# Performance work log

Hardware: AMD Instinct MI355X
Metric: run time of the kernel (lower is better)

Reference implementation:

```python
import jax, jax.numpy as jnp
import numpy as np

N, F_IN, H, OUT = 8192, 512, 128, 3
DEG_P = 16.0 / N  # avg degree ~16


def setup_inputs() -> dict:
    key = jax.random.key(0)
    ks = jax.random.split(key, 10)
    x = jax.random.normal(ks[0], (N, F_IN), dtype=jnp.float32)
    adj = (jax.random.uniform(ks[1], (N, N)) < DEG_P).astype(jnp.float32)

    def glorot(k, shape):
        lim = float(np.sqrt(6.0 / (shape[0] + shape[1])))
        return jax.random.uniform(k, shape, jnp.float32, -lim, lim)

    return {
        "x": x,
        "adj": adj,
        "Wl1": glorot(ks[2], (F_IN, H)),   # neighbor-agg weight, layer 1
        "Wr1": glorot(ks[3], (F_IN, H)),   # root/self weight, layer 1
        "b1": jnp.zeros((H,), jnp.float32),
        "Wl2": glorot(ks[4], (H, H)),
        "Wr2": glorot(ks[5], (H, H)),
        "b2": jnp.zeros((H,), jnp.float32),
        "Wd": glorot(ks[6], (H, OUT)),
        "bd": jnp.zeros((OUT,), jnp.float32),
    }


def _sage(x, adj, Wl, Wr, b):
    # GraphSAGE-mean: mean over neighbors via dense adjacency, then transform.
    deg = jnp.maximum(adj.sum(axis=1, keepdims=True), 1.0)  # [N,1]
    agg = (adj @ x) / deg                                    # [N,F]
    return agg @ Wl + x @ Wr + b


def _cdist(y):
    # pairwise Euclidean distances, grad-safe sqrt (zero grad on zero dist)
    sq = jnp.sum(y * y, axis=-1)                             # [N]
    d2 = jnp.maximum(sq[:, None] + sq[None, :] - 2.0 * (y @ y.T), 0.0)
    return jnp.where(d2 > 0, jnp.sqrt(jnp.where(d2 > 0, d2, 1.0)), 0.0)


def reference(x, adj, Wl1, Wr1, b1, Wl2, Wr2, b2, Wd, bd):
    h = jax.nn.relu(_sage(x, adj, Wl1, Wr1, b1))
    # dropout p=0.5 is identity in eval mode
    h = _sage(h, adj, Wl2, Wr2, b2)
    y = h @ Wd + bd                                          # [N,3]
    return _cdist(y)                                         # [N,N]
```

## Files before the change

### kernel.cpp

```cpp
#include <hip/hip_runtime.h>
#include <math.h>

#define NN 8192
#define FIN 512
#define HD 128
#define CAP 128
#define GEMM_B 512
#define ADJ_B  2048

__global__ __launch_bounds__(256) void k_front(
    const float* __restrict__ x, const float* __restrict__ Wl1,
    const float* __restrict__ Wr1, const float* __restrict__ adj,
    const float* __restrict__ Wl2, const float* __restrict__ Wr2,
    const float* __restrict__ b2, const float* __restrict__ Wd,
    const float* __restrict__ bd,
    float* __restrict__ xl, float* __restrict__ xr,
    int* __restrict__ nbr, int* __restrict__ degi, float* __restrict__ degf,
    float4* __restrict__ wsm)
{
    __shared__ float As[32][32];
    __shared__ float Bs[32][128];
    const int tid = threadIdx.x;

    if (blockIdx.x < GEMM_B) {
        const float* W = (blockIdx.x < 256) ? Wl1 : Wr1;
        float* Cout    = (blockIdx.x < 256) ? xl  : xr;
        const int row0 = (blockIdx.x & 255) * 32;
        const int rg = tid >> 5, cg = tid & 31;
        const int ar = tid >> 3, ak = (tid & 7) * 4;
        const int bk = tid >> 5, bc = (tid & 31) * 4;
        float acc[4][4] = {};
        for (int ch = 0; ch < FIN / 32; ++ch) {
            const int kc = ch * 32;
            __syncthreads();
            const float4 va = *(const float4*)(x + (size_t)(row0 + ar) * FIN + kc + ak);
            As[ak + 0][ar] = va.x; As[ak + 1][ar] = va.y;
            As[ak + 2][ar] = va.z; As[ak + 3][ar] = va.w;
            #pragma unroll
            for (int it = 0; it < 4; ++it)
                *(float4*)&Bs[bk + 8 * it][bc] =
                    *(const float4*)(W + (size_t)(kc + bk + 8 * it) * HD + bc);
            __syncthreads();
            #pragma unroll
            for (int k = 0; k < 32; ++k) {
                const float4 a4 = *(const float4*)&As[k][rg * 4];
                const float4 b4 = *(const float4*)&Bs[k][cg * 4];
                const float av[4] = {a4.x, a4.y, a4.z, a4.w};
                const float bv[4] = {b4.x, b4.y, b4.z, b4.w};
                #pragma unroll
                for (int a = 0; a < 4; ++a)
                    #pragma unroll
                    for (int b = 0; b < 4; ++b)
                        acc[a][b] = fmaf(av[a], bv[b], acc[a][b]);
            }
        }
        #pragma unroll
        for (int a = 0; a < 4; ++a)
            *(float4*)(Cout + (size_t)(row0 + rg * 4 + a) * HD + cg * 4) =
                make_float4(acc[a][0], acc[a][1], acc[a][2], acc[a][3]);
    } else if (blockIdx.x < GEMM_B + ADJ_B) {
        const int w = tid >> 6, lane = tid & 63;
        const int i = (blockIdx.x - GEMM_B) * 4 + w;
        int* lst = nbr + (size_t)i * CAP;
        const float4* row = (const float4*)(adj + (size_t)i * NN);
        const unsigned long long lmask = (1ull << lane) - 1ull;
        int cnt = 0;
        for (int it = 0; it < NN / 256; ++it) {
            const float4 a = row[it * 64 + lane];
            const float vals[4] = {a.x, a.y, a.z, a.w};
            #pragma unroll
            for (int e = 0; e < 4; ++e) {
                const bool nz = (vals[e] != 0.0f);
                const unsigned long long m = __ballot(nz);
                if (nz) {
                    const int p = cnt + (int)__popcll(m & lmask);
                    if (p < CAP) lst[p] = (it * 64 + lane) * 4 + e;
                }
                cnt += (int)__popcll(m);
            }
        }
        if (lane == 0) {
            degi[i] = cnt < CAP ? cnt : CAP;
            degf[i] = fmaxf((float)cnt, 1.0f);
        }
    } else {
        const int t = tid;
        if (t < HD) {
            float l0 = 0, l1 = 0, l2 = 0, r0 = 0, r1 = 0, r2 = 0;
            for (int c = 0; c < HD; ++c) {
                const float w0 = Wd[c * 3 + 0], w1 = Wd[c * 3 + 1], w2 = Wd[c * 3 + 2];
                const float wl = Wl2[t * HD + c];
                const float wr = Wr2[t * HD + c];
                l0 = fmaf(wl, w0, l0); l1 = fmaf(wl, w1, l1); l2 = fmaf(wl, w2, l2);
                r0 = fmaf(wr, w0, r0); r1 = fmaf(wr, w1, r1); r2 = fmaf(wr, w2, r2);
            }
            wsm[t]       = make_float4(l0, l1, l2, 0.f);
            wsm[128 + t] = make_float4(r0, r1, r2, 0.f);
            if (t == 0) {
                float c0 = bd[0], c1 = bd[1], c2 = bd[2];
                for (int c = 0; c < HD; ++c) {
                    c0 = fmaf(b2[c], Wd[c * 3 + 0], c0);
                    c1 = fmaf(b2[c], Wd[c * 3 + 1], c1);
                    c2 = fmaf(b2[c], Wd[c * 3 + 2], c2);
                }
                wsm[256] = make_float4(c0, c1, c2, 0.f);
            }
        }
    }
}

__global__ __launch_bounds__(256) void k_agg_proj(
    const float* __restrict__ xl, const float* __restrict__ xr,
    const float* __restrict__ b1, const int* __restrict__ nbr,
    const int* __restrict__ degi, const float* __restrict__ degf,
    const float4* __restrict__ wsm, float4* __restrict__ u4,
    float4* __restrict__ v4)
{
    __shared__ int lists[4][CAP];
    const int w = threadIdx.x >> 6, lane = threadIdx.x & 63;
    const int i = blockIdx.x * 4 + w;
    const int d = degi[i];
    const float inv = 1.0f / degf[i];
    const int* glst = nbr + (size_t)i * CAP;
    if (lane < d)      lists[w][lane]      = glst[lane];
    if (lane + 64 < d) lists[w][lane + 64] = glst[lane + 64];
    const int* lst = lists[w];

    float s0 = 0.f, s1 = 0.f;
    int t = 0;
    for (; t + 4 <= d; t += 4) {
        const int j0 = lst[t], j1 = lst[t + 1], j2 = lst[t + 2], j3 = lst[t + 3];
        const float2 a0 = ((const float2*)(xl + (size_t)j0 * HD))[lane];
        const float2 a1 = ((const float2*)(xl + (size_t)j1 * HD))[lane];
        const float2 a2 = ((const float2*)(xl + (size_t)j2 * HD))[lane];
        const float2 a3 = ((const float2*)(xl + (size_t)j3 * HD))[lane];
        s0 += a0.x + a1.x + a2.x + a3.x;
        s1 += a0.y + a1.y + a2.y + a3.y;
    }
    for (; t < d; ++t) {
        const float2 a0 = ((const float2*)(xl + (size_t)lst[t] * HD))[lane];
        s0 += a0.x; s1 += a0.y;
    }

    const float2 rr = ((const float2*)(xr + (size_t)i * HD))[lane];
    const float2 bb = ((const float2*)b1)[lane];
    const float h0 = fmaxf(fmaf(s0, inv, rr.x + bb.x), 0.f);
    const float h1 = fmaxf(fmaf(s1, inv, rr.y + bb.y), 0.f);
    const float4 w0 = wsm[2 * lane], w1 = wsm[2 * lane + 1];
    const float4 q0 = wsm[128 + 2 * lane], q1 = wsm[128 + 2 * lane + 1];
    float u0 = h0 * w0.x + h1 * w1.x;
    float u1 = h0 * w0.y + h1 * w1.y;
    float u2 = h0 * w0.z + h1 * w1.z;
    float v0 = h0 * q0.x + h1 * q1.x;
    float v1 = h0 * q0.y + h1 * q1.y;
    float v2 = h0 * q0.z + h1 * q1.z;
    #pragma unroll
    for (int off = 32; off; off >>= 1) {
        u0 += __shfl_xor(u0, off); u1 += __shfl_xor(u1, off); u2 += __shfl_xor(u2, off);
        v0 += __shfl_xor(v0, off); v1 += __shfl_xor(v1, off); v2 += __shfl_xor(v2, off);
    }
    if (lane == 0) {
        u4[i] = make_float4(u0, u1, u2, 0.f);
        v4[i] = make_float4(v0, v1, v2, 0.f);
    }
}

__global__ __launch_bounds__(256) void k_ycomb(
    const float4* __restrict__ u4, const float4* __restrict__ v4,
    const int* __restrict__ nbr, const int* __restrict__ degi,
    const float* __restrict__ degf, const float4* __restrict__ wsm,
    float4* __restrict__ y4)
{
    const int hw = threadIdx.x >> 5;
    const int lane = threadIdx.x & 31;
    const int i = blockIdx.x * 8 + hw;
    const int d = degi[i];
    const float inv = 1.0f / degf[i];
    const int* lst = nbr + (size_t)i * CAP;
    float s0 = 0.f, s1 = 0.f, s2 = 0.f;
    for (int base = 0; base + lane < d; base += 32) {
        const float4 u = u4[lst[base + lane]];
        s0 += u.x; s1 += u.y; s2 += u.z;
    }
    #pragma unroll
    for (int off = 16; off; off >>= 1) {
        s0 += __shfl_xor(s0, off); s1 += __shfl_xor(s1, off); s2 += __shfl_xor(s2, off);
    }
    if (lane == 0) {
        const float4 v = v4[i];
        const float4 c = wsm[256];
        y4[i] = make_float4(fmaf(s0, inv, v.x + c.x),
                            fmaf(s1, inv, v.y + c.y),
                            fmaf(s2, inv, v.z + c.z), 0.f);
    }
}

__global__ __launch_bounds__(256) void k_cdist(
    const float4* __restrict__ y4, float* __restrict__ out)
{
    __shared__ float4 yis[32];
    const int t = threadIdx.x;
    const int i0 = blockIdx.y * 32;
    if (t < 32) yis[t] = y4[i0 + t];
    __syncthreads();
    const int j0 = blockIdx.x * 1024 + t * 4;
    const float4 a0 = y4[j0 + 0], a1 = y4[j0 + 1];
    const float4 a2 = y4[j0 + 2], a3 = y4[j0 + 3];
    float* op = out + (size_t)i0 * NN + j0;
    #pragma unroll 4
    for (int ii = 0; ii < 32; ++ii) {
        const float4 yi = yis[ii];
        float4 r;
        { const float dx = yi.x - a0.x, dy = yi.y - a0.y, dz = yi.z - a0.z;
          r.x = sqrtf(fmaf(dx, dx, fmaf(dy, dy, dz * dz))); }
        { const float dx = yi.x - a1.x, dy = yi.y - a1.y, dz = yi.z - a1.z;
          r.y = sqrtf(fmaf(dx, dx, fmaf(dy, dy, dz * dz))); }
        { const float dx = yi.x - a2.x, dy = yi.y - a2.y, dz = yi.z - a2.z;
          r.z = sqrtf(fmaf(dx, dx, fmaf(dy, dy, dz * dz))); }
        { const float dx = yi.x - a3.x, dy = yi.y - a3.y, dz = yi.z - a3.z;
          r.w = sqrtf(fmaf(dx, dx, fmaf(dy, dy, dz * dz))); }
        *(float4*)op = r;
        op += NN;
    }
}

extern "C" void kernel_launch(void* const* d_in, const int* in_sizes, int n_in,
                              void* d_out, int out_size, void* d_ws, size_t ws_size,
                              hipStream_t stream) {
    const float* x   = (const float*)d_in[0];
    const float* adj = (const float*)d_in[1];
    const float* Wl1 = (const float*)d_in[2];
    const float* Wr1 = (const float*)d_in[3];
    const float* b1  = (const float*)d_in[4];
    const float* Wl2 = (const float*)d_in[5];
    const float* Wr2 = (const float*)d_in[6];
    const float* b2  = (const float*)d_in[7];
    const float* Wd  = (const float*)d_in[8];
    const float* bd  = (const float*)d_in[9];
    float* out = (float*)d_out;

    char* ws = (char*)d_ws;
    const size_t nbr_b  = (size_t)NN * CAP * 4;
    const size_t deg_b  = (size_t)NN * 4;
    const size_t vec_b  = (size_t)NN * 16;
    const size_t wsm_b  = 272 * 16;
    const size_t small_total = nbr_b + 2 * deg_b + 3 * vec_b + wsm_b;
    const size_t xl_b = (size_t)NN * HD * 4;

    size_t off = 0;
    int*    nbr  = (int*)(ws + off);    off += nbr_b;
    int*    degi = (int*)(ws + off);    off += deg_b;
    float*  degf = (float*)(ws + off);  off += deg_b;
    float4* u4   = (float4*)(ws + off); off += vec_b;
    float4* v4   = (float4*)(ws + off); off += vec_b;
    float4* y4   = (float4*)(ws + off); off += vec_b;
    float4* wsm  = (float4*)(ws + off); off += wsm_b;

    char* big = (ws_size >= small_total + 2 * xl_b) ? (ws + off) : (char*)d_out;
    float* xl = (float*)(big);
    float* xr = (float*)(big + xl_b);

    k_front<<<GEMM_B + ADJ_B + 1, 256, 0, stream>>>(
        x, Wl1, Wr1, adj, Wl2, Wr2, b2, Wd, bd,
        xl, xr, nbr, degi, degf, wsm);

    k_agg_proj<<<NN / 4, 256, 0, stream>>>(xl, xr, b1, nbr, degi, degf,
                                           wsm, u4, v4);

    k_ycomb<<<NN / 8, 256, 0, stream>>>(u4, v4, nbr, degi, degf, wsm, y4);

    k_cdist<<<dim3(NN / 1024, NN / 32), 256, 0, stream>>>(y4, out);
}
```

Measured before the change: 146.9 us.

## Fuse all four stages into one persistent cooperative kernel with grid syncs

Adds a persistent cooperative kernel that runs the layer-1 GEMM, adjacency compaction, aggregation/projection, y combination and cdist in a single launch, separated by grid-wide barriers. The goal is to remove three kernel launch gaps and tail effects between stages. The GEMM is also changed to compute Wl1 and Wr1 in the same tile pass so x is loaded once. The risks are the cost of grid syncs, a fixed persistent grid that may give worse load balance, and extra host attribute and occupancy queries on every call. The old multi-kernel path is kept as a fallback.

```diff
diff --git a/kernel.cpp b/kernel.cpp
--- a/kernel.cpp
+++ b/kernel.cpp
@@ -1,5 +1,8 @@
 #include <hip/hip_runtime.h>
+#include <hip/hip_cooperative_groups.h>
 #include <math.h>
+
+namespace cg = cooperative_groups;
 
 #define NN 8192
 #define FIN 512
@@ -7,6 +10,233 @@
 #define CAP 128
 #define GEMM_B 512
 #define ADJ_B  2048
+
+__global__ __launch_bounds__(256, 4) void k_mono(
+    const float* __restrict__ x, const float* __restrict__ Wl1,
+    const float* __restrict__ Wr1, const float* __restrict__ adj,
+    const float* __restrict__ b1, const float* __restrict__ Wl2,
+    const float* __restrict__ Wr2, const float* __restrict__ b2,
+    const float* __restrict__ Wd, const float* __restrict__ bd,
+    float* __restrict__ xl, float* __restrict__ xr,
+    int* __restrict__ nbr, int* __restrict__ degi, float* __restrict__ degf,
+    float4* __restrict__ u4, float4* __restrict__ v4, float4* __restrict__ y4,
+    float4* __restrict__ wsm, float* __restrict__ out)
+{
+    __shared__ union {
+        struct { float As[32][32]; float Bl[32][128]; float Br[32][128]; } g;
+        int lists[4][CAP];
+        float4 yis[32];
+    } sh;
+
+    cg::grid_group gg = cg::this_grid();
+    const int tid = threadIdx.x;
+    const int bid = blockIdx.x;
+    const int nb  = gridDim.x;
+    const int GB  = (nb / 2 < 256) ? nb / 2 : 256;
+
+    if (bid < GB) {
+        const int rg = tid >> 5, cg2 = tid & 31;
+        const int ar = tid >> 3, ak = (tid & 7) * 4;
+        const int bk = tid >> 5, bc = (tid & 31) * 4;
+        for (int t = bid; t < NN / 32; t += GB) {
+            const int row0 = t * 32;
+            float accl[4][4] = {}, accr[4][4] = {};
+            for (int ch = 0; ch < FIN / 32; ++ch) {
+                const int kc = ch * 32;
+                __syncthreads();
+                const float4 va = *(const float4*)(x + (size_t)(row0 + ar) * FIN + kc + ak);
+                sh.g.As[ak + 0][ar] = va.x; sh.g.As[ak + 1][ar] = va.y;
+                sh.g.As[ak + 2][ar] = va.z; sh.g.As[ak + 3][ar] = va.w;
+                #pragma unroll
+                for (int it = 0; it < 4; ++it) {
+                    *(float4*)&sh.g.Bl[bk + 8 * it][bc] =
+                        *(const float4*)(Wl1 + (size_t)(kc + bk + 8 * it) * HD + bc);
+                    *(float4*)&sh.g.Br[bk + 8 * it][bc] =
+                        *(const float4*)(Wr1 + (size_t)(kc + bk + 8 * it) * HD + bc);
+                }
+                __syncthreads();
+                #pragma unroll
+                for (int k = 0; k < 32; ++k) {
+                    const float4 a4  = *(const float4*)&sh.g.As[k][rg * 4];
+                    const float4 bl4 = *(const float4*)&sh.g.Bl[k][cg2 * 4];
+                    const float4 br4 = *(const float4*)&sh.g.Br[k][cg2 * 4];
+                    const float av[4]  = {a4.x, a4.y, a4.z, a4.w};
+                    const float blv[4] = {bl4.x, bl4.y, bl4.z, bl4.w};
+                    const float brv[4] = {br4.x, br4.y, br4.z, br4.w};
+                    #pragma unroll
+                    for (int a = 0; a < 4; ++a)
+                        #pragma unroll
+                        for (int b = 0; b < 4; ++b) {
+                            accl[a][b] = fmaf(av[a], blv[b], accl[a][b]);
+                            accr[a][b] = fmaf(av[a], brv[b], accr[a][b]);
+                        }
+                }
+            }
+            #pragma unroll
+            for (int a = 0; a < 4; ++a) {
+                *(float4*)(xl + (size_t)(row0 + rg * 4 + a) * HD + cg2 * 4) =
+                    make_float4(accl[a][0], accl[a][1], accl[a][2], accl[a][3]);
+                *(float4*)(xr + (size_t)(row0 + rg * 4 + a) * HD + cg2 * 4) =
+                    make_float4(accr[a][0], accr[a][1], accr[a][2], accr[a][3]);
+            }
+        }
+    } else {
+        const int w = tid >> 6, lane = tid & 63;
+        const unsigned long long lmask = (1ull << lane) - 1ull;
+        for (int u = bid - GB; u < NN / 4; u += nb - GB) {
+            const int i = u * 4 + w;
+            int* lst = nbr + (size_t)i * CAP;
+            const float4* row = (const float4*)(adj + (size_t)i * NN);
+            int cnt = 0;
+            for (int it = 0; it < NN / 256; ++it) {
+                const float4 a = row[it * 64 + lane];
+                const float vals[4] = {a.x, a.y, a.z, a.w};
+                #pragma unroll
+                for (int e = 0; e < 4; ++e) {
+                    const bool nz = (vals[e] != 0.0f);
+                    const unsigned long long m = __ballot(nz);
+                    if (nz) {
+                        const int p = cnt + (int)__popcll(m & lmask);
+                        if (p < CAP) lst[p] = (it * 64 + lane) * 4 + e;
+                    }
+                    cnt += (int)__popcll(m);
+                }
+            }
+            if (lane == 0) {
+                degi[i] = cnt < CAP ? cnt : CAP;
+                degf[i] = fmaxf((float)cnt, 1.0f);
+            }
+        }
+        if (bid == nb - 1 && tid < HD) {
+            const int t = tid;
+            float l0 = 0, l1 = 0, l2 = 0, r0 = 0, r1 = 0, r2 = 0;
+            for (int c = 0; c < HD; ++c) {
+                const float w0 = Wd[c * 3 + 0], w1 = Wd[c * 3 + 1], w2 = Wd[c * 3 + 2];
+                const float wl = Wl2[t * HD + c];
+                const float wr = Wr2[t * HD + c];
+                l0 = fmaf(wl, w0, l0); l1 = fmaf(wl, w1, l1); l2 = fmaf(wl, w2, l2);
+                r0 = fmaf(wr, w0, r0); r1 = fmaf(wr, w1, r1); r2 = fmaf(wr, w2, r2);
+            }
+            wsm[t]       = make_float4(l0, l1, l2, 0.f);
+            wsm[128 + t] = make_float4(r0, r1, r2, 0.f);
+            if (t == 0) {
+                float c0 = bd[0], c1 = bd[1], c2 = bd[2];
+                for (int c = 0; c < HD; ++c) {
+                    c0 = fmaf(b2[c], Wd[c * 3 + 0], c0);
+                    c1 = fmaf(b2[c], Wd[c * 3 + 1], c1);
+                    c2 = fmaf(b2[c], Wd[c * 3 + 2], c2);
+                }
+                wsm[256] = make_float4(c0, c1, c2, 0.f);
+            }
+        }
+    }
+    gg.sync();
+
+    {
+        const int w = tid >> 6, lane = tid & 63;
+        int* lst = sh.lists[w];
+        for (int q = bid; q < NN / 4; q += nb) {
+            const int i = q * 4 + w;
+            const int d = degi[i];
+            const float inv = 1.0f / degf[i];
+            const int* glst = nbr + (size_t)i * CAP;
+            if (lane < d)      lst[lane]      = glst[lane];
+            if (lane + 64 < d) lst[lane + 64] = glst[lane + 64];
+
+            float s0 = 0.f, s1 = 0.f;
+            int t = 0;
+            for (; t + 4 <= d; t += 4) {
+                const int j0 = lst[t], j1 = lst[t + 1], j2 = lst[t + 2], j3 = lst[t + 3];
+                const float2 a0 = ((const float2*)(xl + (size_t)j0 * HD))[lane];
+                const float2 a1 = ((const float2*)(xl + (size_t)j1 * HD))[lane];
+                const float2 a2 = ((const float2*)(xl + (size_t)j2 * HD))[lane];
+                const float2 a3 = ((const float2*)(xl + (size_t)j3 * HD))[lane];
+                s0 += a0.x + a1.x + a2.x + a3.x;
+                s1 += a0.y + a1.y + a2.y + a3.y;
+            }
+            for (; t < d; ++t) {
+                const float2 a0 = ((const float2*)(xl + (size_t)lst[t] * HD))[lane];
+                s0 += a0.x; s1 += a0.y;
+            }
+
+            const float2 rr = ((const float2*)(xr + (size_t)i * HD))[lane];
+            const float2 bb = ((const float2*)b1)[lane];
+            const float h0 = fmaxf(fmaf(s0, inv, rr.x + bb.x), 0.f);
+            const float h1 = fmaxf(fmaf(s1, inv, rr.y + bb.y), 0.f);
+            const float4 w0 = wsm[2 * lane], w1 = wsm[2 * lane + 1];
+            const float4 q0 = wsm[128 + 2 * lane], q1 = wsm[128 + 2 * lane + 1];
+            float u0 = h0 * w0.x + h1 * w1.x;
+            float u1 = h0 * w0.y + h1 * w1.y;
+            float u2 = h0 * w0.z + h1 * w1.z;
+            float v0 = h0 * q0.x + h1 * q1.x;
+            float v1 = h0 * q0.y + h1 * q1.y;
+            float v2 = h0 * q0.z + h1 * q1.z;
+            #pragma unroll
+            for (int off = 32; off; off >>= 1) {
+                u0 += __shfl_xor(u0, off); u1 += __shfl_xor(u1, off); u2 += __shfl_xor(u2, off);
+                v0 += __shfl_xor(v0, off); v1 += __shfl_xor(v1, off); v2 += __shfl_xor(v2, off);
+            }
+            if (lane == 0) {
+                u4[i] = make_float4(u0, u1, u2, 0.f);
+                v4[i] = make_float4(v0, v1, v2, 0.f);
+            }
+        }
+    }
+    gg.sync();
+
+    {
+        const int hw = tid >> 5, lane = tid & 31;
+        for (int q = bid; q < NN / 8; q += nb) {
+            const int i = q * 8 + hw;
+            const int d = degi[i];
+            const float inv = 1.0f / degf[i];
+            const int* lst = nbr + (size_t)i * CAP;
+            float s0 = 0.f, s1 = 0.f, s2 = 0.f;
+            for (int base = 0; base + lane < d; base += 32) {
+                const float4 u = u4[lst[base + lane]];
+                s0 += u.x; s1 += u.y; s2 += u.z;
+            }
+            #pragma unroll
+            for (int off = 16; off; off >>= 1) {
+                s0 += __shfl_xor(s0, off); s1 += __shfl_xor(s1, off); s2 += __shfl_xor(s2, off);
+            }
+            if (lane == 0) {
+                const float4 v = v4[i];
+                const float4 c = wsm[256];
+                y4[i] = make_float4(fmaf(s0, inv, v.x + c.x),
+                                    fmaf(s1, inv, v.y + c.y),
+                                    fmaf(s2, inv, v.z + c.z), 0.f);
+            }
+        }
+    }
+    gg.sync();
+
+    for (int t = bid; t < (NN / 32) * (NN / 1024); t += nb) {
+        const int i0 = (t >> 3) * 32;
+        const int jb = (t & 7) * 1024 + tid * 4;
+        __syncthreads();
+        if (tid < 32) sh.yis[tid] = y4[i0 + tid];
+        __syncthreads();
+        const float4 a0 = y4[jb + 0], a1 = y4[jb + 1];
+        const float4 a2 = y4[jb + 2], a3 = y4[jb + 3];
+        float* op = out + (size_t)i0 * NN + jb;
+        #pragma unroll 4
+        for (int ii = 0; ii < 32; ++ii) {
+            const float4 yi = sh.yis[ii];
+            float4 r;
+            { const float dx = yi.x - a0.x, dy = yi.y - a0.y, dz = yi.z - a0.z;
+              r.x = sqrtf(fmaf(dx, dx, fmaf(dy, dy, dz * dz))); }
+            { const float dx = yi.x - a1.x, dy = yi.y - a1.y, dz = yi.z - a1.z;
+              r.y = sqrtf(fmaf(dx, dx, fmaf(dy, dy, dz * dz))); }
+            { const float dx = yi.x - a2.x, dy = yi.y - a2.y, dz = yi.z - a2.z;
+              r.z = sqrtf(fmaf(dx, dx, fmaf(dy, dy, dz * dz))); }
+            { const float dx = yi.x - a3.x, dy = yi.y - a3.y, dz = yi.z - a3.z;
+              r.w = sqrtf(fmaf(dx, dx, fmaf(dy, dy, dz * dz))); }
+            *(float4*)op = r;
+            op += NN;
+        }
+    }
+}
 
 __global__ __launch_bounds__(256) void k_front(
     const float* __restrict__ x, const float* __restrict__ Wl1,
@@ -255,19 +485,42 @@
     float4* v4   = (float4*)(ws + off); off += vec_b;
     float4* y4   = (float4*)(ws + off); off += vec_b;
     float4* wsm  = (float4*)(ws + off); off += wsm_b;
-
     char* big = (ws_size >= small_total + 2 * xl_b) ? (ws + off) : (char*)d_out;
     float* xl = (float*)(big);
     float* xr = (float*)(big + xl_b);
 
+    int dev = 0;
+    (void)hipGetDevice(&dev);
+    int coop = 0;
+    (void)hipDeviceGetAttribute(&coop, hipDeviceAttributeCooperativeLaunch, dev);
+    int ncu = 0;
+    (void)hipDeviceGetAttribute(&ncu, hipDeviceAttributeMultiprocessorCount, dev);
+    if (ncu <= 0) ncu = 256;
+    int maxb = 0;
+    if (coop) {
+        if (hipOccupancyMaxActiveBlocksPerMultiprocessor(&maxb, k_mono, 256, 0)
+            != hipSuccess) maxb = 0;
+    }
+    long grid = (long)maxb * ncu;
+    if (grid > 1024) grid = 1024;
+
+    if (coop && grid >= 512) {
+        void* args[] = {
+            (void*)&x, (void*)&Wl1, (void*)&Wr1, (void*)&adj, (void*)&b1,
+            (void*)&Wl2, (void*)&Wr2, (void*)&b2, (void*)&Wd, (void*)&bd,
+            (void*)&xl, (void*)&xr, (void*)&nbr, (void*)&degi, (void*)&degf,
+            (void*)&u4, (void*)&v4, (void*)&y4, (void*)&wsm, (void*)&out
+        };
+        hipError_t e = hipLaunchCooperativeKernel(
+            k_mono, dim3((unsigned)grid), dim3(256), args, 0u, stream);
+        if (e == hipSuccess) return;
+    }
+
     k_front<<<GEMM_B + ADJ_B + 1, 256, 0, stream>>>(
         x, Wl1, Wr1, adj, Wl2, Wr2, b2, Wd, bd,
         xl, xr, nbr, degi, degf, wsm);
-
     k_agg_proj<<<NN / 4, 256, 0, stream>>>(xl, xr, b1, nbr, degi, degf,
                                            wsm, u4, v4);
-
     k_ycomb<<<NN / 8, 256, 0, stream>>>(u4, v4, nbr, degi, degf, wsm, y4);
-
     k_cdist<<<dim3(NN / 1024, NN / 32), 256, 0, stream>>>(y4, out);
 }
```

After: 418.7 us. +185.1%, slower.
